# Optimization experiments

Hardware: AMD Instinct MI355X
Metric: run time of the kernel (lower is better)

Reference implementation:

```python
import jax, jax.numpy as jnp
import numpy as np

D_MODEL = 1024
HEADS = 16
D_K = D_MODEL // HEADS
D_FF = 4096
B, S = 4, 2048
EPS = 1e-5


def _layer_norm(x, gamma, beta):
    mu = jnp.mean(x, axis=-1, keepdims=True)
    var = jnp.mean(jnp.square(x - mu), axis=-1, keepdims=True)
    return (x - mu) * jax.lax.rsqrt(var + EPS) * gamma + beta


def setup_inputs() -> dict:
    key = jax.random.key(0)
    ks = jax.random.split(key, 16)
    s_in = 1.0 / np.sqrt(D_MODEL)
    s_ff = 1.0 / np.sqrt(D_FF)
    inp = {
        "x": jax.random.normal(ks[0], (B, S, D_MODEL), dtype=jnp.float32),
        "src_mask": jnp.ones((B, 1, 1, S), dtype=jnp.int32),
        "Wq": jax.random.uniform(ks[1], (D_MODEL, D_MODEL), jnp.float32, -s_in, s_in),
        "bq": jnp.zeros((D_MODEL,), jnp.float32),
        "Wk": jax.random.uniform(ks[2], (D_MODEL, D_MODEL), jnp.float32, -s_in, s_in),
        "bk": jnp.zeros((D_MODEL,), jnp.float32),
        "Wv": jax.random.uniform(ks[3], (D_MODEL, D_MODEL), jnp.float32, -s_in, s_in),
        "bv": jnp.zeros((D_MODEL,), jnp.float32),
        "Wo": jax.random.uniform(ks[4], (D_MODEL, D_MODEL), jnp.float32, -s_in, s_in),
        "bo": jnp.zeros((D_MODEL,), jnp.float32),
        "W1": jax.random.uniform(ks[5], (D_MODEL, D_FF), jnp.float32, -s_in, s_in),
        "b1": jnp.zeros((D_FF,), jnp.float32),
        "W2": jax.random.uniform(ks[6], (D_FF, D_MODEL), jnp.float32, -s_ff, s_ff),
        "b2": jnp.zeros((D_MODEL,), jnp.float32),
        "g1": jnp.ones((D_MODEL,), jnp.float32),
        "be1": jnp.zeros((D_MODEL,), jnp.float32),
        "g2": jnp.ones((D_MODEL,), jnp.float32),
        "be2": jnp.zeros((D_MODEL,), jnp.float32),
    }
    return inp


def reference(x, src_mask, Wq, bq, Wk, bk, Wv, bv, Wo, bo, W1, b1, W2, b2, g1, be1, g2, be2):
    Bn, L, _ = x.shape
    # Self-attention (dropout=0 / eval)
    q = (x @ Wq + bq).reshape(Bn, L, HEADS, D_K).transpose(0, 2, 1, 3)  # [B,H,L,dk]
    k = (x @ Wk + bk).reshape(Bn, L, HEADS, D_K).transpose(0, 2, 1, 3)
    v = (x @ Wv + bv).reshape(Bn, L, HEADS, D_K).transpose(0, 2, 1, 3)
    scores = jnp.einsum("bhqd,bhkd->bhqk", q, k) / np.sqrt(D_K).astype(np.float32)
    scores = jnp.where(src_mask == 0, -jnp.inf, scores)
    attn = jax.nn.softmax(scores, axis=-1)
    out = jnp.einsum("bhqk,bhkd->bhqd", attn, v)
    out = out.transpose(0, 2, 1, 3).reshape(Bn, L, D_MODEL)
    attn_out = out @ Wo + bo
    x = _layer_norm(x + attn_out, g1, be1)
    # FFN
    ffn = jax.nn.relu(x @ W1 + b1) @ W2 + b2
    x = _layer_norm(x + ffn, g2, be2)
    return x
```

## Files before the change

kernel.cpp:

```cpp
#include <hip/hip_runtime.h>
#include <hip/hip_bf16.h>
#include <cstdint>
#include <cstddef>

typedef __bf16 bf16;
typedef __bf16 bf16x8 __attribute__((ext_vector_type(8)));
typedef float  f32x4  __attribute__((ext_vector_type(4)));
typedef unsigned short u16x4 __attribute__((ext_vector_type(4)));
typedef uint32_t u32x4 __attribute__((ext_vector_type(4)));

static constexpr int D_MODEL = 1024;
static constexpr int HEADS   = 16;
static constexpr int D_KH    = 64;
static constexpr int D_FF    = 4096;
static constexpr int BATCH   = 4;
static constexpr int SEQ     = 2048;
static constexpr int MROWS   = BATCH * SEQ;
static constexpr float QSCALE = 0.18033688011f;

#define VMCNT(n) asm volatile("s_waitcnt vmcnt(" #n ")" ::: "memory")
#define LGKM0()                                            \
  do {                                                     \
    asm volatile("s_waitcnt lgkmcnt(0)" ::: "memory");     \
    __builtin_amdgcn_sched_barrier(0);                     \
  } while (0)

__device__ __forceinline__ unsigned short bfbits(float f) {
  return __builtin_bit_cast(unsigned short, (bf16)f);
}
__device__ __forceinline__ float bf2f(unsigned short u) {
  return __builtin_bit_cast(float, (uint32_t)u << 16);
}
__device__ __forceinline__ float exp2_raw(float x) {
  float r;
  asm("v_exp_f32 %0, %1" : "=v"(r) : "v"(x));
  return r;
}

__device__ __forceinline__ void gload_lds16(const void* g, void* l) {
  __builtin_amdgcn_global_load_lds(
      (__attribute__((address_space(1))) uint32_t*)(uintptr_t)g,
      (__attribute__((address_space(3))) uint32_t*)(uintptr_t)l, 16, 0, 0);
}

struct PrepArgs {
  const float* x; bf16* xb;
  const int* mask; uint32_t* flags;
  const float* w1; const float* w2; const float* wx[4];
  bf16* w1t; bf16* w2t; bf16* wxt[4];
};
__global__ void k_prep(PrepArgs p) {
  __shared__ float tile[64][65];
  const int t = blockIdx.x;
  if (t < 4096) {
    int i = (t * 256 + threadIdx.x) * 8;
    const float4* q = (const float4*)(p.x + i);
    float4 a = q[0], b = q[1];
    bf16x8 v;
    v[0] = (bf16)a.x; v[1] = (bf16)a.y; v[2] = (bf16)a.z; v[3] = (bf16)a.w;
    v[4] = (bf16)b.x; v[5] = (bf16)b.y; v[6] = (bf16)b.z; v[7] = (bf16)b.w;
    *(bf16x8*)(p.xb + i) = v;
    return;
  }
  if (t == 4096) {
    __shared__ uint32_t sb[4];
    int tid = threadIdx.x;
    if (tid < 4) sb[tid] = 0;
    __syncthreads();
    if (tid < 128) {
      int b = tid >> 5, tt = tid & 31;
      const int4* q = (const int4*)(p.mask + b * SEQ + tt * 64);
      int all = 1;
#pragma unroll
      for (int i = 0; i < 16; ++i) {
        int4 v = q[i];
        all &= v.x & v.y & v.z & v.w;
      }
      if (all) atomicOr(&sb[b], 1u << tt);
    }
    __syncthreads();
    if (tid < 4) p.flags[tid] = sb[tid];
    return;
  }
  int u = t - 4097;
  const float* W;
  bf16* Wt;
  int K, N, k0, n0;
  if (u < 1024) {
    W = p.w1; Wt = p.w1t; K = 1024; N = 4096;
    k0 = (u & 15) * 64; n0 = (u >> 4) * 64;
  } else if (u < 2048) {
    int v = u - 1024;
    W = p.w2; Wt = p.w2t; K = 4096; N = 1024;
    k0 = (v & 63) * 64; n0 = (v >> 6) * 64;
  } else {
    int v = u - 2048;
    int which = v >> 8, vv = v & 255;
    W = p.wx[which]; Wt = p.wxt[which]; K = 1024; N = 1024;
    k0 = (vv & 15) * 64; n0 = (vv >> 4) * 64;
  }
  int c = threadIdx.x & 63, r0 = threadIdx.x >> 6;
#pragma unroll
  for (int i = 0; i < 16; ++i) {
    int r = r0 + i * 4;
    tile[r][c] = W[(size_t)(k0 + r) * N + n0 + c];
  }
  __syncthreads();
#pragma unroll
  for (int i = 0; i < 16; ++i) {
    int r = r0 + i * 4;
    Wt[(size_t)(n0 + r) * K + k0 + c] = (bf16)tile[c][r];
  }
}

enum { EP_RELU = 0, EP_O16 = 1, EP_QKV = 2 };

template <int EPI, int NREP>
__global__ __launch_bounds__(512, 2) void k_gemm8(
    const bf16* __restrict__ A, const bf16* __restrict__ Bt,
    const float* __restrict__ bias, const float* __restrict__ bias2,
    const float* __restrict__ bias3,
    void* __restrict__ Cout, void* __restrict__ C2, void* __restrict__ C3,
    int N, int K) {
  extern __shared__ char smem[];
  constexpr int BN = NREP * 64;
  constexpr int HB = NREP / 2;
  const int tid = threadIdx.x;
  const int lane = tid & 63;
  const int wid = tid >> 6;
  const int wm = wid >> 2, wn = wid & 3;
  const int l15 = lane & 15, l4 = lane >> 4;
  const int bx = blockIdx.x, by = blockIdx.y;
  const int NI = K >> 7;

  const int c0 = tid, c1 = tid + 512;
  const bf16* baseA0 = A + (size_t)(bx * 256 + (c0 >> 3)) * K + ((c0 & 7) ^ ((c0 >> 3) & 7)) * 8;
  const bf16* baseA1 = A + (size_t)(bx * 256 + (c1 >> 3)) * K + ((c1 & 7) ^ ((c1 >> 3) & 7)) * 8;
  const bf16* baseB0 = Bt + (size_t)(by * BN + (c0 >> 3)) * K + ((c0 & 7) ^ ((c0 >> 3) & 7)) * 8;
  const bf16* baseB1 = Bt + (size_t)(by * BN + (c1 >> 3)) * K + ((c1 & 7) ^ ((c1 >> 3) & 7)) * 8;
  const size_t rowK128 = (size_t)128 * K;

  auto stA = [&](int h, int t, int buf) {
    gload_lds16(baseA0 + h * rowK128 + t * 64, smem + buf * 32768 + h * 16384 + c0 * 16);
    gload_lds16(baseA1 + h * rowK128 + t * 64, smem + buf * 32768 + h * 16384 + c1 * 16);
  };
  auto stB = [&](int h, int t, int buf) {
    gload_lds16(baseB0 + h * rowK128 + t * 64,
                smem + 65536 + buf * (HB * 16384) + h * 16384 + c0 * 16);
    gload_lds16(baseB1 + h * rowK128 + t * 64,
                smem + 65536 + buf * (HB * 16384) + h * 16384 + c1 * 16);
  };

  const int ch0 = (l4 ^ (l15 & 7)) * 16;
  const int ch1 = ((4 + l4) ^ (l15 & 7)) * 16;
  const int aoff = l15 * 128;
  int boffh[NREP];
#pragma unroll
  for (int n = 0; n < NREP; ++n) {
    int rB = wn * (NREP * 16) + n * 16 + l15;
    boffh[n] = (rB >> 7) * 16384 + (rB & 127) * 128;
  }

  f32x4 acc[8][NREP] = {};
  bf16x8 breg[NREP][2];

  stA(0, 0, 0); stA(1, 0, 0); stB(0, 0, 0);
  if constexpr (HB == 2) stB(1, 0, 0);
  stA(0, 1, 1); stA(1, 1, 1); stB(0, 1, 1);
  if constexpr (HB == 2) stB(1, 1, 1);

  for (int i = 0; i < NI; ++i) {
    const int t1 = 2 * i + 1, t2 = 2 * i + 2;
    const bool notfirst = (i > 0), notlast = (i + 1 < NI);
#pragma unroll
    for (int p = 0; p < 8; ++p) {
      const int q = p & 3;
      const char* Ab = smem + (p >> 2) * 32768 + wm * 16384;
      const char* Bb = smem + 65536 + (p >> 2) * (HB * 16384);
      if (p == 0) {
        if (notfirst) {
          stA(0, t1, 1);
          VMCNT(2);
        } else {
          if constexpr (HB == 2) VMCNT(8); else VMCNT(6);
        }
        __builtin_amdgcn_s_barrier();
      } else if (p == 4) {
        if (notlast) {
          stA(0, t2, 0);
          VMCNT(2);
        } else {
          VMCNT(0);
        }
        __builtin_amdgcn_s_barrier();
      }
      if (q == 0) {
#pragma unroll
        for (int n = 0; n < NREP; ++n) {
          breg[n][0] = *(const bf16x8*)(Bb + boffh[n] + ch0);
          breg[n][1] = *(const bf16x8*)(Bb + boffh[n] + ch1);
        }
      }
      bf16x8 a0k0 = *(const bf16x8*)(Ab + (2 * q + 0) * 2048 + aoff + ch0);
      bf16x8 a0k1 = *(const bf16x8*)(Ab + (2 * q + 0) * 2048 + aoff + ch1);
      bf16x8 a1k0 = *(const bf16x8*)(Ab + (2 * q + 1) * 2048 + aoff + ch0);
      bf16x8 a1k1 = *(const bf16x8*)(Ab + (2 * q + 1) * 2048 + aoff + ch1);
      if (p == 1) { if (notfirst) stA(1, t1, 1); }
      else if (p == 2) { if (notfirst) stB(0, t1, 1); }
      else if (p == 3) { if constexpr (HB == 2) { if (notfirst) stB(1, t1, 1); } }
      else if (p == 5) { if (notlast) stA(1, t2, 0); }
      else if (p == 6) { if (notlast) stB(0, t2, 0); }
      else if (p == 7) { if constexpr (HB == 2) { if (notlast) stB(1, t2, 0); } }
      if (p != 0 && p != 4) __builtin_amdgcn_s_barrier();
      LGKM0();
      __builtin_amdgcn_s_setprio(1);
#pragma unroll
      for (int n = 0; n < NREP; ++n) {
        acc[2 * q + 0][n] = __builtin_amdgcn_mfma_f32_16x16x32_bf16(a0k0, breg[n][0], acc[2 * q + 0][n], 0, 0, 0);
        acc[2 * q + 0][n] = __builtin_amdgcn_mfma_f32_16x16x32_bf16(a0k1, breg[n][1], acc[2 * q + 0][n], 0, 0, 0);
        acc[2 * q + 1][n] = __builtin_amdgcn_mfma_f32_16x16x32_bf16(a1k0, breg[n][0], acc[2 * q + 1][n], 0, 0, 0);
        acc[2 * q + 1][n] = __builtin_amdgcn_mfma_f32_16x16x32_bf16(a1k1, breg[n][1], acc[2 * q + 1][n], 0, 0, 0);
      }
      __builtin_amdgcn_s_setprio(0);
      __builtin_amdgcn_s_barrier();
    }
  }

  constexpr int BPM = 1024 / BN;
  float bia[NREP];
#pragma unroll
  for (int n = 0; n < NREP; ++n) {
    int colL = wn * (NREP * 16) + n * 16 + l15;
    if constexpr (EPI == EP_QKV) {
      const int g = by / BPM;
      const float* bp = (g == 0) ? bias : (g == 1 ? bias2 : bias3);
      bia[n] = bp[(by % BPM) * BN + colL];
    } else {
      bia[n] = bias[by * BN + colL];
    }
  }
#pragma unroll
  for (int mf = 0; mf < 8; ++mf) {
    int row0 = bx * 256 + wm * 128 + mf * 16 + l4 * 4;
#pragma unroll
    for (int n = 0; n < NREP; ++n) {
      int colL = wn * (NREP * 16) + n * 16 + l15;
      if constexpr (EPI == EP_QKV) {
        const int g = by / BPM;
        int cc = (by % BPM) * BN + colL;
        if (g == 2) {
          int bidx = row0 >> 11, s0 = row0 & 2047;
          u16x4 pk;
#pragma unroll
          for (int r = 0; r < 4; ++r) pk[r] = bfbits(acc[mf][n][r] + bia[n]);
          *(u16x4*)((bf16*)C3 + (((size_t)bidx * HEADS + (cc >> 6)) * D_KH + (cc & 63)) * SEQ + s0) = pk;
        } else if (g == 0) {
          bf16* dst = (bf16*)Cout;
#pragma unroll
          for (int r = 0; r < 4; ++r)
            dst[(size_t)(row0 + r) * 1024 + cc] = (bf16)((acc[mf][n][r] + bia[n]) * QSCALE);
        } else {
          bf16* dst = (bf16*)C2;
#pragma unroll
          for (int r = 0; r < 4; ++r)
            dst[(size_t)(row0 + r) * 1024 + cc] = (bf16)(acc[mf][n][r] + bia[n]);
        }
      } else {
        int col = by * BN + colL;
#pragma unroll
        for (int r = 0; r < 4; ++r) {
          float v = acc[mf][n][r] + bia[n];
          if constexpr (EPI == EP_RELU) v = fmaxf(v, 0.f);
          ((bf16*)Cout)[(size_t)(row0 + r) * N + col] = (bf16)v;
        }
      }
    }
  }
}

__global__ __launch_bounds__(256, 4) void k_attn(
    const bf16* __restrict__ Q, const bf16* __restrict__ Kb,
    const bf16* __restrict__ Vt, const int* __restrict__ mask,
    const uint32_t* __restrict__ Mf, bf16* __restrict__ O) {
  __shared__ bf16 Ks[2][64 * 64];
  __shared__ bf16 Vs[2][64 * 64];
  const int tid = threadIdx.x;
  const int lane = tid & 63;
  const int l15 = lane & 15, l4 = lane >> 4;
  const int L = blockIdx.x;
  const int xcd = L & 7, rest = L >> 3;
  const int qx = rest & 15, yhi = rest >> 4;
  const int bh = yhi * 8 + xcd;
  const int b = bh >> 4, h = bh & 15;
  const size_t qrow0 = (size_t)b * SEQ + qx * 128 + (tid >> 6) * 32;
  const bf16* Kbase = Kb + (size_t)b * SEQ * D_MODEL + h * 64;
  const bf16* Vbase = Vt + (size_t)bh * D_KH * SEQ;
  const int* mbase = mask + b * SEQ;
  const uint32_t mflags = Mf[b];

  bf16x8 qf[2][2];
#pragma unroll
  for (int m = 0; m < 2; ++m)
#pragma unroll
    for (int ks = 0; ks < 2; ++ks)
      qf[m][ks] = *(const bf16x8*)&Q[(qrow0 + m * 16 + l15) * D_MODEL + h * 64 + ks * 32 + l4 * 8];

  f32x4 o[2][4] = {};
  f32x4 rs[2] = {};
  bf16x8 ones;
#pragma unroll
  for (int i = 0; i < 8; ++i) ones[i] = (bf16)1.0f;

  const int koff0 = l15 * 64 + ((l4 * 8) ^ ((l15 & 7) << 3));
  const int koff1 = l15 * 64 + ((32 + l4 * 8) ^ ((l15 & 7) << 3));

  const int r0_ = tid >> 3, c0_ = (tid & 7) ^ (r0_ & 7);
  const int o1_ = tid + 256;
  const int r1_ = o1_ >> 3, c1_ = (o1_ & 7) ^ (r1_ & 7);
  const bf16* gK0 = Kbase + (size_t)r0_ * D_MODEL + c0_ * 8;
  const bf16* gK1 = Kbase + (size_t)r1_ * D_MODEL + c1_ * 8;
  const bf16* gV0 = Vbase + (size_t)r0_ * SEQ + c0_ * 8;
  const bf16* gV1 = Vbase + (size_t)r1_ * SEQ + c1_ * 8;
  char* ldsK = (char*)&Ks[0][0] + tid * 16;
  char* ldsV = (char*)&Vs[0][0] + tid * 16;

  auto stage = [&](int buf) {
    gload_lds16(gK0, ldsK + buf * 8192);
    gload_lds16(gK1, ldsK + buf * 8192 + 4096);
    gload_lds16(gV0, ldsV + buf * 8192);
    gload_lds16(gV1, ldsV + buf * 8192 + 4096);
    gK0 += 64 * D_MODEL; gK1 += 64 * D_MODEL;
    gV0 += 64; gV1 += 64;
  };

  stage(0);
  __syncthreads();

  for (int kv0 = 0; kv0 < SEQ; kv0 += 64) {
    const int cur = (kv0 >> 6) & 1;
    if (kv0 + 64 < SEQ) stage(cur ^ 1);
    const bf16* Kc = &Ks[cur][0];
    const bf16* Vc = &Vs[cur][0];

    f32x4 sf[2][4] = {};
    __builtin_amdgcn_s_setprio(1);
#pragma unroll
    for (int ks = 0; ks < 2; ++ks)
#pragma unroll
      for (int n = 0; n < 4; ++n) {
        bf16x8 kf = *(const bf16x8*)&Kc[(ks ? koff1 : koff0) + n * 1024];
#pragma unroll
        for (int m = 0; m < 2; ++m)
          sf[m][n] = __builtin_amdgcn_mfma_f32_16x16x32_bf16(kf, qf[m][ks], sf[m][n], 0, 0, 0);
      }
    __builtin_amdgcn_s_setprio(0);

    if (__builtin_expect(!((mflags >> (kv0 >> 6)) & 1), 0)) {
#pragma unroll
      for (int n = 0; n < 4; ++n) {
        int4 mk = *(const int4*)&mbase[kv0 + n * 16 + l4 * 4];
#pragma unroll
        for (int r = 0; r < 4; ++r)
          if (((const int*)&mk)[r] == 0) {
            sf[0][n][r] = -1e30f;
            sf[1][n][r] = -1e30f;
          }
      }
    }

    uint32_t pk[2][4][2];
#pragma unroll
    for (int m = 0; m < 2; ++m) {
#pragma unroll
      for (int n = 0; n < 4; ++n) {
#pragma unroll
        for (int r = 0; r < 4; ++r) sf[m][n][r] = exp2_raw(sf[m][n][r]);
        asm("v_cvt_pk_bf16_f32 %0, %1, %2"
            : "=v"(pk[m][n][0]) : "v"(sf[m][n][0]), "v"(sf[m][n][1]));
        asm("v_cvt_pk_bf16_f32 %0, %1, %2"
            : "=v"(pk[m][n][1]) : "v"(sf[m][n][2]), "v"(sf[m][n][3]));
      }
    }

    bf16x8 pa[2][2];
#pragma unroll
    for (int m = 0; m < 2; ++m)
#pragma unroll
      for (int ks = 0; ks < 2; ++ks) {
        u32x4 w;
#pragma unroll
        for (int hh = 0; hh < 2; ++hh) {
          uint32_t a = pk[m][ks * 2 + 0][hh];
          uint32_t bsw = pk[m][ks * 2 + 1][hh];
          asm("v_permlane32_swap_b32 %0, %1" : "+v"(a), "+v"(bsw));
          asm("v_permlane16_swap_b32 %0, %1" : "+v"(a), "+v"(bsw));
          w[hh] = a;
          w[2 + hh] = bsw;
        }
        pa[ks][m] = __builtin_bit_cast(bf16x8, w);
      }

#pragma unroll
    for (int ks = 0; ks < 2; ++ks) {
      __builtin_amdgcn_s_setprio(1);
#pragma unroll
      for (int n = 0; n < 4; ++n) {
        bf16x8 vf = *(const bf16x8*)&Vc[(ks ? koff1 : koff0) + n * 1024];
#pragma unroll
        for (int m = 0; m < 2; ++m)
          o[m][n] = __builtin_amdgcn_mfma_f32_16x16x32_bf16(pa[ks][m], vf, o[m][n], 0, 0, 0);
      }
#pragma unroll
      for (int m = 0; m < 2; ++m)
        rs[m] = __builtin_amdgcn_mfma_f32_16x16x32_bf16(pa[ks][m], ones, rs[m], 0, 0, 0);
      __builtin_amdgcn_s_setprio(0);
    }
    __syncthreads();
  }

#pragma unroll
  for (int m = 0; m < 2; ++m) {
    float inv[4];
#pragma unroll
    for (int r = 0; r < 4; ++r) inv[r] = 1.0f / rs[m][r];
#pragma unroll
    for (int n = 0; n < 4; ++n)
#pragma unroll
      for (int r = 0; r < 4; ++r)
        O[(qrow0 + m * 16 + l4 * 4 + r) * D_MODEL + h * 64 + n * 16 + l15] =
            (bf16)(o[m][n][r] * inv[r]);
  }
}

__global__ __launch_bounds__(256) void k_add_ln1(
    const bf16* __restrict__ a, const bf16* __restrict__ b,
    const float* __restrict__ g, const float* __restrict__ be,
    bf16* __restrict__ y) {
  const int t = threadIdx.x;
  const size_t base = (size_t)blockIdx.x * D_MODEL + t * 4;
  u16x4 va = *(const u16x4*)(a + base);
  u16x4 vb = *(const u16x4*)(b + base);
  float v0 = bf2f(va[0]) + bf2f(vb[0]), v1 = bf2f(va[1]) + bf2f(vb[1]);
  float v2 = bf2f(va[2]) + bf2f(vb[2]), v3 = bf2f(va[3]) + bf2f(vb[3]);
  float s  = v0 + v1 + v2 + v3;
  float s2 = v0 * v0 + v1 * v1 + v2 * v2 + v3 * v3;
#pragma unroll
  for (int off = 1; off < 64; off <<= 1) {
    s  += __shfl_xor(s, off);
    s2 += __shfl_xor(s2, off);
  }
  __shared__ float red1[4], red2[4];
  int w = t >> 6;
  if ((t & 63) == 0) { red1[w] = s; red2[w] = s2; }
  __syncthreads();
  s  = red1[0] + red1[1] + red1[2] + red1[3];
  s2 = red2[0] + red2[1] + red2[2] + red2[3];
  float mu  = s * (1.f / D_MODEL);
  float var = s2 * (1.f / D_MODEL) - mu * mu;
  float rstd = rsqrtf(var + 1e-5f);
  float4 vg  = *(const float4*)(g + t * 4);
  float4 vbe = *(const float4*)(be + t * 4);
  u16x4 pk = {bfbits((v0 - mu) * rstd * vg.x + vbe.x),
              bfbits((v1 - mu) * rstd * vg.y + vbe.y),
              bfbits((v2 - mu) * rstd * vg.z + vbe.z),
              bfbits((v3 - mu) * rstd * vg.w + vbe.w)};
  *(u16x4*)(y + base) = pk;
}

__global__ __launch_bounds__(256) void k_add_ln2(
    const bf16* __restrict__ a, const bf16* __restrict__ b,
    const float* __restrict__ g, const float* __restrict__ be,
    float* __restrict__ y) {
  const int t = threadIdx.x;
  const size_t base = (size_t)blockIdx.x * D_MODEL + t * 4;
  u16x4 va = *(const u16x4*)(a + base);
  u16x4 vb = *(const u16x4*)(b + base);
  float v0 = bf2f(va[0]) + bf2f(vb[0]), v1 = bf2f(va[1]) + bf2f(vb[1]);
  float v2 = bf2f(va[2]) + bf2f(vb[2]), v3 = bf2f(va[3]) + bf2f(vb[3]);
  float s  = v0 + v1 + v2 + v3;
  float s2 = v0 * v0 + v1 * v1 + v2 * v2 + v3 * v3;
#pragma unroll
  for (int off = 1; off < 64; off <<= 1) {
    s  += __shfl_xor(s, off);
    s2 += __shfl_xor(s2, off);
  }
  __shared__ float red1[4], red2[4];
  int w = t >> 6;
  if ((t & 63) == 0) { red1[w] = s; red2[w] = s2; }
  __syncthreads();
  s  = red1[0] + red1[1] + red1[2] + red1[3];
  s2 = red2[0] + red2[1] + red2[2] + red2[3];
  float mu  = s * (1.f / D_MODEL);
  float var = s2 * (1.f / D_MODEL) - mu * mu;
  float rstd = rsqrtf(var + 1e-5f);
  float4 vg  = *(const float4*)(g + t * 4);
  float4 vbe = *(const float4*)(be + t * 4);
  *(float4*)(y + base) = make_float4((v0 - mu) * rstd * vg.x + vbe.x,
                                     (v1 - mu) * rstd * vg.y + vbe.y,
                                     (v2 - mu) * rstd * vg.z + vbe.z,
                                     (v3 - mu) * rstd * vg.w + vbe.w);
}

extern "C" void kernel_launch(void* const* d_in, const int* in_sizes, int n_in,
                              void* d_out, int out_size, void* d_ws, size_t ws_size,
                              hipStream_t stream) {
  const float* x   = (const float*)d_in[0];
  const int*  mask = (const int*)d_in[1];
  const float* Wq  = (const float*)d_in[2];
  const float* bq  = (const float*)d_in[3];
  const float* Wk  = (const float*)d_in[4];
  const float* bk_ = (const float*)d_in[5];
  const float* Wv  = (const float*)d_in[6];
  const float* bv  = (const float*)d_in[7];
  const float* Wo  = (const float*)d_in[8];
  const float* bo  = (const float*)d_in[9];
  const float* W1  = (const float*)d_in[10];
  const float* b1  = (const float*)d_in[11];
  const float* W2  = (const float*)d_in[12];
  const float* b2  = (const float*)d_in[13];
  const float* g1  = (const float*)d_in[14];
  const float* be1 = (const float*)d_in[15];
  const float* g2  = (const float*)d_in[16];
  const float* be2 = (const float*)d_in[17];

  char* ws = (char*)d_ws;
  const size_t MB = 1ull << 20;
  bf16*  xb    = (bf16*)(ws + 0);
  bf16*  Qb    = (bf16*)(ws + 16 * MB);
  bf16*  Kbuf  = (bf16*)(ws + 32 * MB);
  bf16*  Vt    = (bf16*)(ws + 48 * MB);
  bf16*  Hb    = (bf16*)(ws + 0);
  bf16*  aproj = (bf16*)(ws + 64 * MB);
  bf16*  f2o   = (bf16*)(ws + 80 * MB);
  bf16*  Ob    = (bf16*)(ws + 96 * MB);
  uint32_t* mfl = (uint32_t*)(ws + 112 * MB);
  bf16*  x1b   = (bf16*)(ws + 128 * MB);
  bf16*  Wqkvt = (bf16*)(ws + 144 * MB);
  bf16*  Wot   = (bf16*)(ws + 150 * MB);
  bf16*  W1t   = (bf16*)(ws + 152 * MB);
  bf16*  W2t   = (bf16*)(ws + 160 * MB);

  const int SM4 = 131072, SM2 = 98304;
  hipFuncSetAttribute(reinterpret_cast<const void*>(&k_gemm8<EP_QKV, 2>),
                      hipFuncAttributeMaxDynamicSharedMemorySize, SM2);
  hipFuncSetAttribute(reinterpret_cast<const void*>(&k_gemm8<EP_RELU, 4>),
                      hipFuncAttributeMaxDynamicSharedMemorySize, SM4);
  hipFuncSetAttribute(reinterpret_cast<const void*>(&k_gemm8<EP_O16, 2>),
                      hipFuncAttributeMaxDynamicSharedMemorySize, SM2);

  PrepArgs pp;
  pp.x = x; pp.xb = xb; pp.mask = mask; pp.flags = mfl;
  pp.w1 = W1; pp.w1t = W1t;
  pp.w2 = W2; pp.w2t = W2t;
  pp.wx[0] = Wq; pp.wxt[0] = Wqkvt;
  pp.wx[1] = Wk; pp.wxt[1] = Wqkvt + 1024 * 1024;
  pp.wx[2] = Wv; pp.wxt[2] = Wqkvt + 2 * 1024 * 1024;
  pp.wx[3] = Wo; pp.wxt[3] = Wot;
  k_prep<<<7169, 256, 0, stream>>>(pp);

  k_gemm8<EP_QKV, 2><<<dim3(32, 24), 512, SM2, stream>>>(
      xb, Wqkvt, bq, bk_, bv, Qb, Kbuf, Vt, 3072, 1024);

  k_attn<<<1024, 256, 0, stream>>>(Qb, Kbuf, Vt, mask, mfl, Ob);

  k_gemm8<EP_O16, 2><<<dim3(32, 8), 512, SM2, stream>>>(
      Ob, Wot, bo, nullptr, nullptr, aproj, nullptr, nullptr, 1024, 1024);
  k_add_ln1<<<MROWS, 256, 0, stream>>>(xb, aproj, g1, be1, x1b);

  k_gemm8<EP_RELU, 4><<<dim3(32, 16), 512, SM4, stream>>>(
      x1b, W1t, b1, nullptr, nullptr, Hb, nullptr, nullptr, 4096, 1024);
  k_gemm8<EP_O16, 2><<<dim3(32, 8), 512, SM2, stream>>>(
      Hb, W2t, b2, nullptr, nullptr, f2o, nullptr, nullptr, 1024, 4096);
  k_add_ln2<<<MROWS, 256, 0, stream>>>(x1b, f2o, g2, be2, (float*)d_out);
}
```

Before: 325.5 us.

## Switch attention kernel from 16x16x32 to 32x32x16 MFMA tiles

Rewrites the attention inner loop to use 32x32x16 bf16 MFMA instructions instead of 16x16x32, which changes the Q fragment layout, the LDS read offsets, the P repacking (now a single permlane32 swap) and the output indexing. Larger MFMA tiles issue fewer instructions and perform fewer LDS fragment loads per FLOP. The risks are higher accumulator register pressure, which may cut occupancy at 4 blocks per SM, and a changed masking path that now does scalar mask loads.

```diff
diff --git a/kernel.cpp b/kernel.cpp
--- a/kernel.cpp
+++ b/kernel.cpp
@@ -6,6 +6,7 @@
 typedef __bf16 bf16;
 typedef __bf16 bf16x8 __attribute__((ext_vector_type(8)));
 typedef float  f32x4  __attribute__((ext_vector_type(4)));
+typedef float  f32x16 __attribute__((ext_vector_type(16)));
 typedef unsigned short u16x4 __attribute__((ext_vector_type(4)));
 typedef uint32_t u32x4 __attribute__((ext_vector_type(4)));
 
@@ -286,7 +287,7 @@
   __shared__ bf16 Vs[2][64 * 64];
   const int tid = threadIdx.x;
   const int lane = tid & 63;
-  const int l15 = lane & 15, l4 = lane >> 4;
+  const int l31 = lane & 31, hi = lane >> 5;
   const int L = blockIdx.x;
   const int xcd = L & 7, rest = L >> 3;
   const int qx = rest & 15, yhi = rest >> 4;
@@ -298,21 +299,21 @@
   const int* mbase = mask + b * SEQ;
   const uint32_t mflags = Mf[b];
 
-  bf16x8 qf[2][2];
-#pragma unroll
-  for (int m = 0; m < 2; ++m)
-#pragma unroll
-    for (int ks = 0; ks < 2; ++ks)
-      qf[m][ks] = *(const bf16x8*)&Q[(qrow0 + m * 16 + l15) * D_MODEL + h * 64 + ks * 32 + l4 * 8];
-
-  f32x4 o[2][4] = {};
-  f32x4 rs[2] = {};
+  bf16x8 qf[4];
+#pragma unroll
+  for (int st = 0; st < 4; ++st)
+    qf[st] = *(const bf16x8*)&Q[(qrow0 + l31) * D_MODEL + h * 64 + st * 16 + hi * 8];
+
+  f32x16 o0 = {}, o1 = {}, rs = {};
   bf16x8 ones;
 #pragma unroll
   for (int i = 0; i < 8; ++i) ones[i] = (bf16)1.0f;
 
-  const int koff0 = l15 * 64 + ((l4 * 8) ^ ((l15 & 7) << 3));
-  const int koff1 = l15 * 64 + ((32 + l4 * 8) ^ ((l15 & 7) << 3));
+  const int rb0 = l31 * 128;
+  const int swz = l31 & 7;
+  int choff[4];
+#pragma unroll
+  for (int i = 0; i < 4; ++i) choff[i] = ((2 * i + hi) ^ swz) * 16;
 
   const int r0_ = tid >> 3, c0_ = (tid & 7) ^ (r0_ & 7);
   const int o1_ = tid + 256;
@@ -339,96 +340,82 @@
   for (int kv0 = 0; kv0 < SEQ; kv0 += 64) {
     const int cur = (kv0 >> 6) & 1;
     if (kv0 + 64 < SEQ) stage(cur ^ 1);
-    const bf16* Kc = &Ks[cur][0];
-    const bf16* Vc = &Vs[cur][0];
-
-    f32x4 sf[2][4] = {};
+    const char* KcB = (const char*)&Ks[cur][0];
+    const char* VcB = (const char*)&Vs[cur][0];
+
+    f32x16 sf0 = {}, sf1 = {};
     __builtin_amdgcn_s_setprio(1);
 #pragma unroll
-    for (int ks = 0; ks < 2; ++ks)
-#pragma unroll
-      for (int n = 0; n < 4; ++n) {
-        bf16x8 kf = *(const bf16x8*)&Kc[(ks ? koff1 : koff0) + n * 1024];
-#pragma unroll
-        for (int m = 0; m < 2; ++m)
-          sf[m][n] = __builtin_amdgcn_mfma_f32_16x16x32_bf16(kf, qf[m][ks], sf[m][n], 0, 0, 0);
-      }
+    for (int st = 0; st < 4; ++st) {
+      bf16x8 k0 = *(const bf16x8*)(KcB + rb0 + choff[st]);
+      bf16x8 k1 = *(const bf16x8*)(KcB + 4096 + rb0 + choff[st]);
+      sf0 = __builtin_amdgcn_mfma_f32_32x32x16_bf16(k0, qf[st], sf0, 0, 0, 0);
+      sf1 = __builtin_amdgcn_mfma_f32_32x32x16_bf16(k1, qf[st], sf1, 0, 0, 0);
+    }
     __builtin_amdgcn_s_setprio(0);
 
     if (__builtin_expect(!((mflags >> (kv0 >> 6)) & 1), 0)) {
 #pragma unroll
-      for (int n = 0; n < 4; ++n) {
-        int4 mk = *(const int4*)&mbase[kv0 + n * 16 + l4 * 4];
-#pragma unroll
-        for (int r = 0; r < 4; ++r)
-          if (((const int*)&mk)[r] == 0) {
-            sf[0][n][r] = -1e30f;
-            sf[1][n][r] = -1e30f;
-          }
-      }
-    }
-
-    uint32_t pk[2][4][2];
-#pragma unroll
-    for (int m = 0; m < 2; ++m) {
-#pragma unroll
-      for (int n = 0; n < 4; ++n) {
-#pragma unroll
-        for (int r = 0; r < 4; ++r) sf[m][n][r] = exp2_raw(sf[m][n][r]);
-        asm("v_cvt_pk_bf16_f32 %0, %1, %2"
-            : "=v"(pk[m][n][0]) : "v"(sf[m][n][0]), "v"(sf[m][n][1]));
-        asm("v_cvt_pk_bf16_f32 %0, %1, %2"
-            : "=v"(pk[m][n][1]) : "v"(sf[m][n][2]), "v"(sf[m][n][3]));
-      }
-    }
-
-    bf16x8 pa[2][2];
-#pragma unroll
-    for (int m = 0; m < 2; ++m)
-#pragma unroll
-      for (int ks = 0; ks < 2; ++ks) {
-        u32x4 w;
-#pragma unroll
-        for (int hh = 0; hh < 2; ++hh) {
-          uint32_t a = pk[m][ks * 2 + 0][hh];
-          uint32_t bsw = pk[m][ks * 2 + 1][hh];
-          asm("v_permlane32_swap_b32 %0, %1" : "+v"(a), "+v"(bsw));
-          asm("v_permlane16_swap_b32 %0, %1" : "+v"(a), "+v"(bsw));
-          w[hh] = a;
-          w[2 + hh] = bsw;
-        }
-        pa[ks][m] = __builtin_bit_cast(bf16x8, w);
-      }
-
-#pragma unroll
-    for (int ks = 0; ks < 2; ++ks) {
-      __builtin_amdgcn_s_setprio(1);
-#pragma unroll
-      for (int n = 0; n < 4; ++n) {
-        bf16x8 vf = *(const bf16x8*)&Vc[(ks ? koff1 : koff0) + n * 1024];
-#pragma unroll
-        for (int m = 0; m < 2; ++m)
-          o[m][n] = __builtin_amdgcn_mfma_f32_16x16x32_bf16(pa[ks][m], vf, o[m][n], 0, 0, 0);
-      }
-#pragma unroll
-      for (int m = 0; m < 2; ++m)
-        rs[m] = __builtin_amdgcn_mfma_f32_16x16x32_bf16(pa[ks][m], ones, rs[m], 0, 0, 0);
-      __builtin_amdgcn_s_setprio(0);
-    }
+      for (int r = 0; r < 16; ++r) {
+        int kvr = kv0 + (r & 3) + 8 * (r >> 2) + 4 * hi;
+        if (mbase[kvr] == 0) sf0[r] = -1e30f;
+        if (mbase[kvr + 32] == 0) sf1[r] = -1e30f;
+      }
+    }
+
+    uint32_t wpk[2][4][2];
+#pragma unroll
+    for (int r = 0; r < 16; ++r) {
+      sf0[r] = exp2_raw(sf0[r]);
+      sf1[r] = exp2_raw(sf1[r]);
+    }
+#pragma unroll
+    for (int q2 = 0; q2 < 4; ++q2) {
+      asm("v_cvt_pk_bf16_f32 %0, %1, %2"
+          : "=v"(wpk[0][q2][0]) : "v"(sf0[4 * q2 + 0]), "v"(sf0[4 * q2 + 1]));
+      asm("v_cvt_pk_bf16_f32 %0, %1, %2"
+          : "=v"(wpk[0][q2][1]) : "v"(sf0[4 * q2 + 2]), "v"(sf0[4 * q2 + 3]));
+      asm("v_cvt_pk_bf16_f32 %0, %1, %2"
+          : "=v"(wpk[1][q2][0]) : "v"(sf1[4 * q2 + 0]), "v"(sf1[4 * q2 + 1]));
+      asm("v_cvt_pk_bf16_f32 %0, %1, %2"
+          : "=v"(wpk[1][q2][1]) : "v"(sf1[4 * q2 + 2]), "v"(sf1[4 * q2 + 3]));
+    }
+
+    bf16x8 pa[4];
+#pragma unroll
+    for (int j = 0; j < 4; ++j) {
+      int kb = j >> 1, qb = 2 * (j & 1);
+      u32x4 w;
+#pragma unroll
+      for (int hh = 0; hh < 2; ++hh) {
+        uint32_t u = wpk[kb][qb][hh];
+        uint32_t v = wpk[kb][qb + 1][hh];
+        asm("v_permlane32_swap_b32 %0, %1" : "+v"(u), "+v"(v));
+        w[hh] = u;
+        w[2 + hh] = v;
+      }
+      pa[j] = __builtin_bit_cast(bf16x8, w);
+    }
+
+    __builtin_amdgcn_s_setprio(1);
+#pragma unroll
+    for (int j = 0; j < 4; ++j) {
+      bf16x8 v0 = *(const bf16x8*)(VcB + rb0 + choff[j]);
+      bf16x8 v1 = *(const bf16x8*)(VcB + 4096 + rb0 + choff[j]);
+      o0 = __builtin_amdgcn_mfma_f32_32x32x16_bf16(pa[j], v0, o0, 0, 0, 0);
+      o1 = __builtin_amdgcn_mfma_f32_32x32x16_bf16(pa[j], v1, o1, 0, 0, 0);
+      rs = __builtin_amdgcn_mfma_f32_32x32x16_bf16(pa[j], ones, rs, 0, 0, 0);
+    }
+    __builtin_amdgcn_s_setprio(0);
     __syncthreads();
   }
 
 #pragma unroll
-  for (int m = 0; m < 2; ++m) {
-    float inv[4];
-#pragma unroll
-    for (int r = 0; r < 4; ++r) inv[r] = 1.0f / rs[m][r];
-#pragma unroll
-    for (int n = 0; n < 4; ++n)
-#pragma unroll
-      for (int r = 0; r < 4; ++r)
-        O[(qrow0 + m * 16 + l4 * 4 + r) * D_MODEL + h * 64 + n * 16 + l15] =
-            (bf16)(o[m][n][r] * inv[r]);
+  for (int r = 0; r < 16; ++r) {
+    float iv = 1.0f / rs[r];
+    size_t row = (qrow0 + (r & 3) + 8 * (r >> 2) + 4 * hi) * D_MODEL + h * 64;
+    O[row + l31] = (bf16)(o0[r] * iv);
+    O[row + 32 + l31] = (bf16)(o1[r] * iv);
   }
 }
 
```

After: 335.9 us. 3.2% more time.
